# Optimization experiments

Measured on AMD Instinct MI355X. Metric: run time of the kernel, lower is better.

## Reference

```python
import jax, jax.numpy as jnp
import numpy as np

EPS = 1e-7  # undefined global in source; standard small epsilon
LAMBD_BDC = 1.0
LAMBD_BEC = 1.0
N, C = 8192, 100


def setup_inputs() -> dict:
    key = jax.random.key(0)
    k1, k2 = jax.random.split(key)
    inputs = jax.random.normal(k1, (N, C), dtype=jnp.float32)
    targets = jax.random.randint(k2, (N,), 0, C)
    return {"inputs": inputs, "targets": targets}


def _rest_indices(targets, num_classes):
    # Indices of all classes except the target, preserving original class order
    # (matches torch boolean-mask gather ordering).
    idx = jnp.arange(num_classes)[None, :]                 # [1, C]
    is_target = idx == targets[:, None]                    # [N, C]
    # Stable sort: non-target positions first, in ascending class order.
    order = jnp.argsort(is_target, axis=1, stable=True)    # [N, C]
    return order[:, : num_classes - 1]                     # [N, C-1]


def reference(inputs, targets):
    n, c = inputs.shape
    # Cross-entropy (mean reduction, as nn.CrossEntropyLoss default)
    logp = jax.nn.log_softmax(inputs, axis=1)
    loss_ce = -jnp.mean(jnp.take_along_axis(logp, targets[:, None], axis=1))

    # Gather target logit and the C-1 non-target logits per row
    logits_y = jnp.take_along_axis(inputs, targets[:, None], axis=1)   # [N, 1]
    rest_idx = _rest_indices(targets, c)
    logits_rest = jnp.take_along_axis(inputs, rest_idx, axis=1)        # [N, C-1]

    # BDC: -sum(logsigmoid(y - rest)) / (C-1) / N
    loss_bdc = -jnp.sum(jax.nn.log_sigmoid(logits_y - logits_rest)) / (c - 1) / n

    # BEC: pairwise differences among non-target logits, [N, C-1, C-1]
    diff = logits_rest[:, :, None] - logits_rest[:, None, :]
    loss_bec = -jnp.sum(0.5 * jax.nn.log_sigmoid(diff + EPS)) / (c - 1) / (c - 2) / n

    loss = loss_ce + LAMBD_BDC * loss_bdc + LAMBD_BEC * loss_bec
    return (loss, loss_ce, loss_bdc, loss_bec)
```

## Files before the change

kernel.cpp:

```cpp
#include <hip/hip_runtime.h>

#define NROWS 8192
#define NCLS  100
#define NB    (NROWS / 4)
#define LN2   0.6931471805599453f
#define LOG2E 1.4426950408889634f

#if __has_builtin(__builtin_amdgcn_exp2f)
#define EXP2F(x) __builtin_amdgcn_exp2f(x)
#else
#define EXP2F(x) __expf((x) * LN2)
#endif
#if __has_builtin(__builtin_amdgcn_logf)
#define LOG2F(x) __builtin_amdgcn_logf(x)
#else
#define LOG2F(x) (__logf(x) * LOG2E)
#endif

#define TILEIJ(idx, I, J) \
    float s_##I = sqrtf(fmaf(8.f, (float)(idx), 1.f)); \
    int J = (int)((1.0f + s_##I) * 0.5f); \
    int I = (idx) - ((J * (J - 1)) >> 1);

#define HT(EA, RA, EB, RB, P) { P *= fmaf((EB), (RA), (EA) * (RB)); }

#define TILE16H(Ea, Ra, Eb, Rb, P0, P1, P2, P3) \
  HT(Ea.x, Ra.x, Eb.x, Rb.x, P0) HT(Ea.x, Ra.x, Eb.y, Rb.y, P0) \
  HT(Ea.x, Ra.x, Eb.z, Rb.z, P0) HT(Ea.x, Ra.x, Eb.w, Rb.w, P0) \
  HT(Ea.y, Ra.y, Eb.x, Rb.x, P1) HT(Ea.y, Ra.y, Eb.y, Rb.y, P1) \
  HT(Ea.y, Ra.y, Eb.z, Rb.z, P1) HT(Ea.y, Ra.y, Eb.w, Rb.w, P1) \
  HT(Ea.z, Ra.z, Eb.x, Rb.x, P2) HT(Ea.z, Ra.z, Eb.y, Rb.y, P2) \
  HT(Ea.z, Ra.z, Eb.z, Rb.z, P2) HT(Ea.z, Ra.z, Eb.w, Rb.w, P2) \
  HT(Ea.w, Ra.w, Eb.x, Rb.x, P3) HT(Ea.w, Ra.w, Eb.y, Rb.y, P3) \
  HT(Ea.w, Ra.w, Eb.z, Rb.z, P3) HT(Ea.w, Ra.w, Eb.w, Rb.w, P3)

__device__ __forceinline__ float wave_dpp_sum(float v) {
#define DPPADD(ctrl) { int y_ = __builtin_amdgcn_update_dpp( \
        0, __builtin_bit_cast(int, v), (ctrl), 0xf, 0xf, true); \
        v += __builtin_bit_cast(float, y_); }
    DPPADD(0x111)
    DPPADD(0x112)
    DPPADD(0x114)
    DPPADD(0x118)
    DPPADD(0x142)
    DPPADD(0x143)
#undef DPPADD
    return v;
}

__global__ __launch_bounds__(256, 8) void cpc_rows(const float* __restrict__ in,
                                                   const int* __restrict__ tgt,
                                                   float* __restrict__ qb) {
    __shared__ __align__(16) float sx[4][128], sE[4][128], sR[4][128];
    __shared__ float bred[4][3];

    const int tid = threadIdx.x;
    const int w   = tid >> 6;
    const int l   = tid & 63;
    const int row = blockIdx.x * 4 + w;
    const float* x = in + row * NCLS;

    float x0 = x[l] * LOG2E;
    float E0 = EXP2F((x0 - 4.f) * 0.5f);
    sx[w][l] = x0;
    sE[w][l] = E0;
    sR[w][l] = EXP2F((x0 + 4.f) * -0.5f);
    const bool v1 = (l < NCLS - 64);
    float x1 = 0.f, E1 = 0.f;
    if (v1) {
        x1 = x[64 + l] * LOG2E;
        E1 = EXP2F((x1 - 4.f) * 0.5f);
        sx[w][64 + l] = x1;
        sE[w][64 + l] = E1;
        sR[w][64 + l] = EXP2F((x1 + 4.f) * -0.5f);
    }
    __syncthreads();

    const int   t  = tgt[row];
    const float xt = sx[w][t];

    float At, Pb, es, xs;
    {
        float a0 = fabsf(xt - x0);
        float e0 = (l == t) ? 0.f : EXP2F(-a0);
        At = a0; Pb = 1.f + e0;
        es = E0 * E0;
        xs = x0;
    }
    {
        float a1 = v1 ? fabsf(xt - x1) : 0.f;
        float e1 = (v1 && (64 + l) != t) ? EXP2F(-a1) : 0.f;
        At += a1; Pb = fmaf(Pb, e1, Pb);
        es = v1 ? fmaf(E1, E1, es) : es;
        xs += x1;
    }
    float lPb = LOG2F(Pb);

    const float* pE = sE[w];
    const float* pR = sR[w];

    float P0 = 1.f, P1 = 1.f, P2 = 1.f, P3 = 1.f;
    float cst = 512.f;
#pragma unroll 1
    for (int it = 0; it < 4; ++it) {
        int idx = it * 64 + l;
        TILEIJ(idx, I, J)
        float4 Ea = *(const float4*)(pE + 4 * I);
        float4 Ra = *(const float4*)(pR + 4 * I);
        float4 Eb = *(const float4*)(pE + 4 * J);
        float4 Rb = *(const float4*)(pR + 4 * J);
        TILE16H(Ea, Ra, Eb, Rb, P0, P1, P2, P3)
    }
    {
        int idx = 256 + l;
        bool tv = idx < 300;
        int idxc = tv ? idx : 0;
        TILEIJ(idxc, I, J)
        float4 Ea = *(const float4*)(pE + 4 * I);
        float4 Ra = *(const float4*)(pR + 4 * I);
        float4 Eb = *(const float4*)(pE + 4 * J);
        float4 Rb = *(const float4*)(pR + 4 * J);
        float S0 = P0, S1 = P1, S2 = P2, S3 = P3;
        TILE16H(Ea, Ra, Eb, Rb, P0, P1, P2, P3)
        P0 = tv ? P0 : S0; P1 = tv ? P1 : S1;
        P2 = tv ? P2 : S2; P3 = tv ? P3 : S3;
        cst += tv ? 128.f : 0.f;
    }
    float Pd0 = 1.f, Pd1 = 1.f;
    {
        bool dv = l < 25;
        int I = dv ? l : 0;
        float4 Ea = *(const float4*)(pE + 4 * I);
        float4 Ra = *(const float4*)(pR + 4 * I);
        TILE16H(Ea, Ra, Ea, Ra, Pd0, Pd1, Pd0, Pd1)
        Pd0 = dv ? Pd0 : 1.f;
        Pd1 = dv ? Pd1 : 1.f;
        cst += dv ? 64.f : 0.f;
    }

    float lS = 2.f * ((LOG2F(P0) + LOG2F(P1)) + (LOG2F(P2) + LOG2F(P3)))
             + LOG2F(Pd0 * Pd1) + cst;

    float r0 = wave_dpp_sum(es);
    float rU = wave_dpp_sum(xs + At + 2.f * lPb);
    float rW = wave_dpp_sum(At + 2.f * lPb - lS);

    if (l == 63) {
        bred[w][0] = LN2 * (LOG2F(r0) + 4.f - xt);
        bred[w][1] = LN2 * (50.f * xt - 0.5f * rU);
        bred[w][2] = LN2 * (rW + 1.f);
    }
    __syncthreads();
    if (tid < 3) {
        float s = bred[0][tid] + bred[1][tid] + bred[2][tid] + bred[3][tid];
        qb[tid * NB + blockIdx.x] = s;
    }
}

__global__ __launch_bounds__(256) void cpc_final(const float* __restrict__ qb,
                                                 float* __restrict__ out) {
    __shared__ double sred[4][3];
    const int tid = threadIdx.x;
    const int lane = tid & 63, wid = tid >> 6;
    double a0 = 0, a1 = 0, a2 = 0;
#pragma unroll
    for (int it = 0; it < 2; ++it) {
        int idx = (it * 256 + tid) * 4;
        float4 v0 = *(const float4*)(qb + idx);
        float4 v1 = *(const float4*)(qb + NB + idx);
        float4 v2 = *(const float4*)(qb + 2 * NB + idx);
        a0 += (double)v0.x; a0 += (double)v0.y; a0 += (double)v0.z; a0 += (double)v0.w;
        a1 += (double)v1.x; a1 += (double)v1.y; a1 += (double)v1.z; a1 += (double)v1.w;
        a2 += (double)v2.x; a2 += (double)v2.y; a2 += (double)v2.z; a2 += (double)v2.w;
    }
#pragma unroll
    for (int off = 32; off; off >>= 1) {
        a0 += __shfl_xor(a0, off, 64);
        a1 += __shfl_xor(a1, off, 64);
        a2 += __shfl_xor(a2, off, 64);
    }
    if (lane == 0) { sred[wid][0] = a0; sred[wid][1] = a1; sred[wid][2] = a2; }
    __syncthreads();
    if (tid == 0) {
        double ce  = (sred[0][0] + sred[1][0] + sred[2][0] + sred[3][0]) / (double)NROWS;
        double bdc = -(sred[0][1] + sred[1][1] + sred[2][1] + sred[3][1])
                     / (double)(NCLS - 1) / (double)NROWS;
        double bec = -0.5 * (sred[0][2] + sred[1][2] + sred[2][2] + sred[3][2])
                     / (double)(NCLS - 1) / (double)(NCLS - 2) / (double)NROWS;
        out[0] = (float)(ce + bdc + bec);
        out[1] = (float)ce;
        out[2] = (float)bdc;
        out[3] = (float)bec;
    }
}

extern "C" void kernel_launch(void* const* d_in, const int* in_sizes, int n_in,
                              void* d_out, int out_size, void* d_ws, size_t ws_size,
                              hipStream_t stream) {
    const float* inputs  = (const float*)d_in[0];
    const int*   targets = (const int*)d_in[1];
    float*       out     = (float*)d_out;
    float*       qb      = (float*)d_ws;

    cpc_rows<<<NB, 256, 0, stream>>>(inputs, targets, qb);
    cpc_final<<<1, 256, 0, stream>>>(qb, out);
}
```

Before: 14.64 us.

## Process two rows per wave and replace four log2 calls with exponent extraction

Each wave now handles two rows, so blocks cover 8 rows and the grid is halved. Both rows' loads and exp computations are issued before the barrier, which gives more memory-level parallelism per wave. The final reduction then reads half as many partials. The four separate LOG2F calls on the product accumulators are replaced by splitting off the float exponent bits and taking one log of the combined mantissas, which cuts transcendental work. The trade-off is fewer waves in flight (2048 blocks become 1024), longer serial work per wave, and higher LDS use per block.

```diff
diff --git a/kernel.cpp b/kernel.cpp
--- a/kernel.cpp
+++ b/kernel.cpp
@@ -2,7 +2,7 @@
 
 #define NROWS 8192
 #define NCLS  100
-#define NB    (NROWS / 4)
+#define NBLK  (NROWS / 8)
 #define LN2   0.6931471805599453f
 #define LOG2E 1.4426950408889634f
 
@@ -48,112 +48,137 @@
     return v;
 }
 
+#define EXPSPLIT(P, EI, MF) \
+    int   EI = __builtin_bit_cast(int, P) >> 23; \
+    float MF = __builtin_bit_cast(float, (__builtin_bit_cast(int, P) & 0x007FFFFF) | 0x3F800000);
+
 __global__ __launch_bounds__(256, 8) void cpc_rows(const float* __restrict__ in,
                                                    const int* __restrict__ tgt,
                                                    float* __restrict__ qb) {
-    __shared__ __align__(16) float sx[4][128], sE[4][128], sR[4][128];
+    __shared__ __align__(16) float sx[4][2][128], sE[4][2][128], sR[4][2][128];
     __shared__ float bred[4][3];
 
     const int tid = threadIdx.x;
     const int w   = tid >> 6;
     const int l   = tid & 63;
-    const int row = blockIdx.x * 4 + w;
-    const float* x = in + row * NCLS;
-
-    float x0 = x[l] * LOG2E;
-    float E0 = EXP2F((x0 - 4.f) * 0.5f);
-    sx[w][l] = x0;
-    sE[w][l] = E0;
-    sR[w][l] = EXP2F((x0 + 4.f) * -0.5f);
+    const int row0 = blockIdx.x * 8 + w * 2;
+    const float* xA = in + row0 * NCLS;
+    const float* xB = xA + NCLS;
     const bool v1 = (l < NCLS - 64);
-    float x1 = 0.f, E1 = 0.f;
+
+    float xa0 = xA[l] * LOG2E;
+    float xb0 = xB[l] * LOG2E;
+    float Ea0 = EXP2F((xa0 - 4.f) * 0.5f);
+    float Eb0 = EXP2F((xb0 - 4.f) * 0.5f);
+    sx[w][0][l] = xa0; sE[w][0][l] = Ea0; sR[w][0][l] = EXP2F((xa0 + 4.f) * -0.5f);
+    sx[w][1][l] = xb0; sE[w][1][l] = Eb0; sR[w][1][l] = EXP2F((xb0 + 4.f) * -0.5f);
+    float xa1 = 0.f, xb1 = 0.f, Ea1 = 0.f, Eb1 = 0.f;
     if (v1) {
-        x1 = x[64 + l] * LOG2E;
-        E1 = EXP2F((x1 - 4.f) * 0.5f);
-        sx[w][64 + l] = x1;
-        sE[w][64 + l] = E1;
-        sR[w][64 + l] = EXP2F((x1 + 4.f) * -0.5f);
-    }
+        xa1 = xA[64 + l] * LOG2E;
+        xb1 = xB[64 + l] * LOG2E;
+        Ea1 = EXP2F((xa1 - 4.f) * 0.5f);
+        Eb1 = EXP2F((xb1 - 4.f) * 0.5f);
+        sx[w][0][64 + l] = xa1; sE[w][0][64 + l] = Ea1; sR[w][0][64 + l] = EXP2F((xa1 + 4.f) * -0.5f);
+        sx[w][1][64 + l] = xb1; sE[w][1][64 + l] = Eb1; sR[w][1][64 + l] = EXP2F((xb1 + 4.f) * -0.5f);
+    }
+    const int t0 = tgt[row0];
+    const int t1 = tgt[row0 + 1];
     __syncthreads();
 
-    const int   t  = tgt[row];
-    const float xt = sx[w][t];
-
-    float At, Pb, es, xs;
-    {
-        float a0 = fabsf(xt - x0);
-        float e0 = (l == t) ? 0.f : EXP2F(-a0);
-        At = a0; Pb = 1.f + e0;
-        es = E0 * E0;
-        xs = x0;
-    }
-    {
-        float a1 = v1 ? fabsf(xt - x1) : 0.f;
-        float e1 = (v1 && (64 + l) != t) ? EXP2F(-a1) : 0.f;
-        At += a1; Pb = fmaf(Pb, e1, Pb);
-        es = v1 ? fmaf(E1, E1, es) : es;
-        xs += x1;
-    }
-    float lPb = LOG2F(Pb);
-
-    const float* pE = sE[w];
-    const float* pR = sR[w];
-
-    float P0 = 1.f, P1 = 1.f, P2 = 1.f, P3 = 1.f;
-    float cst = 512.f;
+    float acc0 = 0.f, acc1 = 0.f, acc2 = 0.f;
+
 #pragma unroll 1
-    for (int it = 0; it < 4; ++it) {
-        int idx = it * 64 + l;
-        TILEIJ(idx, I, J)
-        float4 Ea = *(const float4*)(pE + 4 * I);
-        float4 Ra = *(const float4*)(pR + 4 * I);
-        float4 Eb = *(const float4*)(pE + 4 * J);
-        float4 Rb = *(const float4*)(pR + 4 * J);
-        TILE16H(Ea, Ra, Eb, Rb, P0, P1, P2, P3)
-    }
-    {
-        int idx = 256 + l;
-        bool tv = idx < 300;
-        int idxc = tv ? idx : 0;
-        TILEIJ(idxc, I, J)
-        float4 Ea = *(const float4*)(pE + 4 * I);
-        float4 Ra = *(const float4*)(pR + 4 * I);
-        float4 Eb = *(const float4*)(pE + 4 * J);
-        float4 Rb = *(const float4*)(pR + 4 * J);
-        float S0 = P0, S1 = P1, S2 = P2, S3 = P3;
-        TILE16H(Ea, Ra, Eb, Rb, P0, P1, P2, P3)
-        P0 = tv ? P0 : S0; P1 = tv ? P1 : S1;
-        P2 = tv ? P2 : S2; P3 = tv ? P3 : S3;
-        cst += tv ? 128.f : 0.f;
-    }
-    float Pd0 = 1.f, Pd1 = 1.f;
-    {
-        bool dv = l < 25;
-        int I = dv ? l : 0;
-        float4 Ea = *(const float4*)(pE + 4 * I);
-        float4 Ra = *(const float4*)(pR + 4 * I);
-        TILE16H(Ea, Ra, Ea, Ra, Pd0, Pd1, Pd0, Pd1)
-        Pd0 = dv ? Pd0 : 1.f;
-        Pd1 = dv ? Pd1 : 1.f;
-        cst += dv ? 64.f : 0.f;
-    }
-
-    float lS = 2.f * ((LOG2F(P0) + LOG2F(P1)) + (LOG2F(P2) + LOG2F(P3)))
-             + LOG2F(Pd0 * Pd1) + cst;
-
-    float r0 = wave_dpp_sum(es);
-    float rU = wave_dpp_sum(xs + At + 2.f * lPb);
-    float rW = wave_dpp_sum(At + 2.f * lPb - lS);
-
-    if (l == 63) {
-        bred[w][0] = LN2 * (LOG2F(r0) + 4.f - xt);
-        bred[w][1] = LN2 * (50.f * xt - 0.5f * rU);
-        bred[w][2] = LN2 * (rW + 1.f);
-    }
+    for (int r = 0; r < 2; ++r) {
+        const float* px = sx[w][r];
+        const float* pE = sE[w][r];
+        const float* pR = sR[w][r];
+        const float x0 = r ? xb0 : xa0;
+        const float x1 = r ? xb1 : xa1;
+        const float E0 = r ? Eb0 : Ea0;
+        const float E1 = r ? Eb1 : Ea1;
+        const int   t  = r ? t1 : t0;
+        const float xt = px[t];
+
+        float At, Pb, es, xs;
+        {
+            float a0 = fabsf(xt - x0);
+            float e0 = (l == t) ? 0.f : EXP2F(-a0);
+            At = a0; Pb = 1.f + e0;
+            es = E0 * E0;
+            xs = x0;
+        }
+        {
+            float a1 = v1 ? fabsf(xt - x1) : 0.f;
+            float e1 = (v1 && (64 + l) != t) ? EXP2F(-a1) : 0.f;
+            At += a1; Pb = fmaf(Pb, e1, Pb);
+            es = v1 ? fmaf(E1, E1, es) : es;
+            xs += x1;
+        }
+        float lPb = LOG2F(Pb);
+
+        float P0 = 1.f, P1 = 1.f, P2 = 1.f, P3 = 1.f;
+        float cst = 512.f;
+#pragma unroll 1
+        for (int it = 0; it < 4; ++it) {
+            int idx = it * 64 + l;
+            TILEIJ(idx, I, J)
+            float4 Ea = *(const float4*)(pE + 4 * I);
+            float4 Ra = *(const float4*)(pR + 4 * I);
+            float4 Eb = *(const float4*)(pE + 4 * J);
+            float4 Rb = *(const float4*)(pR + 4 * J);
+            TILE16H(Ea, Ra, Eb, Rb, P0, P1, P2, P3)
+        }
+        {
+            int idx = 256 + l;
+            bool tv = idx < 300;
+            int idxc = tv ? idx : 0;
+            TILEIJ(idxc, I, J)
+            float4 Ea = *(const float4*)(pE + 4 * I);
+            float4 Ra = *(const float4*)(pR + 4 * I);
+            float4 Eb = *(const float4*)(pE + 4 * J);
+            float4 Rb = *(const float4*)(pR + 4 * J);
+            float S0 = P0, S1 = P1, S2 = P2, S3 = P3;
+            TILE16H(Ea, Ra, Eb, Rb, P0, P1, P2, P3)
+            P0 = tv ? P0 : S0; P1 = tv ? P1 : S1;
+            P2 = tv ? P2 : S2; P3 = tv ? P3 : S3;
+            cst += tv ? 128.f : 0.f;
+        }
+        float Pd0 = 1.f, Pd1 = 1.f;
+        {
+            bool dv = l < 25;
+            int I = dv ? l : 0;
+            float4 Ea = *(const float4*)(pE + 4 * I);
+            float4 Ra = *(const float4*)(pR + 4 * I);
+            TILE16H(Ea, Ra, Ea, Ra, Pd0, Pd1, Pd0, Pd1)
+            Pd0 = dv ? Pd0 : 1.f;
+            Pd1 = dv ? Pd1 : 1.f;
+            cst += dv ? 64.f : 0.f;
+        }
+
+        float Pd = Pd0 * Pd1;
+        EXPSPLIT(P0, e0i, m0) EXPSPLIT(P1, e1i, m1)
+        EXPSPLIT(P2, e2i, m2) EXPSPLIT(P3, e3i, m3)
+        EXPSPLIT(Pd, edi, md)
+        int eAll = 2 * (((e0i + e1i) + (e2i + e3i)) - 508) + (edi - 127);
+        float mA = (m0 * m1) * (m2 * m3);
+        float lS = (float)eAll + LOG2F((mA * mA) * md) + cst;
+
+        float r0 = wave_dpp_sum(es);
+        float rU = wave_dpp_sum(xs + At + 2.f * lPb);
+        float rW = wave_dpp_sum(At + 2.f * lPb - lS);
+
+        if (l == 63) {
+            acc0 += LN2 * (LOG2F(r0) + 4.f - xt);
+            acc1 += LN2 * (50.f * xt - 0.5f * rU);
+            acc2 += LN2 * (rW + 1.f);
+        }
+    }
+
+    if (l == 63) { bred[w][0] = acc0; bred[w][1] = acc1; bred[w][2] = acc2; }
     __syncthreads();
     if (tid < 3) {
         float s = bred[0][tid] + bred[1][tid] + bred[2][tid] + bred[3][tid];
-        qb[tid * NB + blockIdx.x] = s;
+        qb[tid * NBLK + blockIdx.x] = s;
     }
 }
 
@@ -163,12 +188,11 @@
     const int tid = threadIdx.x;
     const int lane = tid & 63, wid = tid >> 6;
     double a0 = 0, a1 = 0, a2 = 0;
-#pragma unroll
-    for (int it = 0; it < 2; ++it) {
-        int idx = (it * 256 + tid) * 4;
+    {
+        int idx = tid * 4;
         float4 v0 = *(const float4*)(qb + idx);
-        float4 v1 = *(const float4*)(qb + NB + idx);
-        float4 v2 = *(const float4*)(qb + 2 * NB + idx);
+        float4 v1 = *(const float4*)(qb + NBLK + idx);
+        float4 v2 = *(const float4*)(qb + 2 * NBLK + idx);
         a0 += (double)v0.x; a0 += (double)v0.y; a0 += (double)v0.z; a0 += (double)v0.w;
         a1 += (double)v1.x; a1 += (double)v1.y; a1 += (double)v1.z; a1 += (double)v1.w;
         a2 += (double)v2.x; a2 += (double)v2.y; a2 += (double)v2.z; a2 += (double)v2.w;
@@ -202,6 +226,6 @@
     float*       out     = (float*)d_out;
     float*       qb      = (float*)d_ws;
 
-    cpc_rows<<<NB, 256, 0, stream>>>(inputs, targets, qb);
+    cpc_rows<<<NBLK, 256, 0, stream>>>(inputs, targets, qb);
     cpc_final<<<1, 256, 0, stream>>>(qb, out);
 }
```

New measurement: 14.75 us. No clear change (+0.8%).

## Compute pairwise BEC products in packed fp16 with interleaved E/R shared layout

Applied to the files above, without the earlier changes.

Stores the exp(x/2) and exp(-x/2) factors as fp16 interleaved in one shared array, so each 4-class tile loads as a single 16-byte h8. The pairwise terms are then computed with packed half2 math and partial products are folded into fewer fp32 accumulators, with the scale offsets and constants changed to match. This is meant to halve shared-memory traffic and the ALU work of the O(C^2) inner loop. In exchange, the reduced fp16 range and precision in the products could affect accuracy or overflow.

```diff
diff --git a/kernel.cpp b/kernel.cpp
--- a/kernel.cpp
+++ b/kernel.cpp
@@ -17,22 +17,32 @@
 #define LOG2F(x) (__logf(x) * LOG2E)
 #endif
 
+typedef _Float16 h2 __attribute__((ext_vector_type(2)));
+typedef _Float16 h8 __attribute__((ext_vector_type(8)));
+
 #define TILEIJ(idx, I, J) \
     float s_##I = sqrtf(fmaf(8.f, (float)(idx), 1.f)); \
     int J = (int)((1.0f + s_##I) * 0.5f); \
     int I = (idx) - ((J * (J - 1)) >> 1);
 
-#define HT(EA, RA, EB, RB, P) { P *= fmaf((EB), (RA), (EA) * (RB)); }
-
-#define TILE16H(Ea, Ra, Eb, Rb, P0, P1, P2, P3) \
-  HT(Ea.x, Ra.x, Eb.x, Rb.x, P0) HT(Ea.x, Ra.x, Eb.y, Rb.y, P0) \
-  HT(Ea.x, Ra.x, Eb.z, Rb.z, P0) HT(Ea.x, Ra.x, Eb.w, Rb.w, P0) \
-  HT(Ea.y, Ra.y, Eb.x, Rb.x, P1) HT(Ea.y, Ra.y, Eb.y, Rb.y, P1) \
-  HT(Ea.y, Ra.y, Eb.z, Rb.z, P1) HT(Ea.y, Ra.y, Eb.w, Rb.w, P1) \
-  HT(Ea.z, Ra.z, Eb.x, Rb.x, P2) HT(Ea.z, Ra.z, Eb.y, Rb.y, P2) \
-  HT(Ea.z, Ra.z, Eb.z, Rb.z, P2) HT(Ea.z, Ra.z, Eb.w, Rb.w, P2) \
-  HT(Ea.w, Ra.w, Eb.x, Rb.x, P3) HT(Ea.w, Ra.w, Eb.y, Rb.y, P3) \
-  HT(Ea.w, Ra.w, Eb.z, Rb.z, P3) HT(Ea.w, Ra.w, Eb.w, Rb.w, P3)
+__device__ __forceinline__ h2 ht2(_Float16 ei, _Float16 ri, h2 EJ, h2 RJ) {
+    h2 e = {ei, ei}, r = {ri, ri};
+    return e * RJ + EJ * r;
+}
+
+#define TILE2x(rI, rJ, PA, PB) { \
+    h2 EJ0 = {rJ[0], rJ[1]}, EJ1 = {rJ[2], rJ[3]}; \
+    h2 RJ0 = {rJ[4], rJ[5]}, RJ1 = {rJ[6], rJ[7]}; \
+    h2 pa = ht2(rI[0], rI[4], EJ0, RJ0); \
+    pa *= ht2(rI[0], rI[4], EJ1, RJ1); \
+    pa *= ht2(rI[1], rI[5], EJ0, RJ0); \
+    pa *= ht2(rI[1], rI[5], EJ1, RJ1); \
+    h2 pb = ht2(rI[2], rI[6], EJ0, RJ0); \
+    pb *= ht2(rI[2], rI[6], EJ1, RJ1); \
+    pb *= ht2(rI[3], rI[7], EJ0, RJ0); \
+    pb *= ht2(rI[3], rI[7], EJ1, RJ1); \
+    PA *= (float)pa[0] * (float)pa[1]; \
+    PB *= (float)pb[0] * (float)pb[1]; }
 
 __device__ __forceinline__ float wave_dpp_sum(float v) {
 #define DPPADD(ctrl) { int y_ = __builtin_amdgcn_update_dpp( \
@@ -51,7 +61,8 @@
 __global__ __launch_bounds__(256, 8) void cpc_rows(const float* __restrict__ in,
                                                    const int* __restrict__ tgt,
                                                    float* __restrict__ qb) {
-    __shared__ __align__(16) float sx[4][128], sE[4][128], sR[4][128];
+    __shared__ float sx[4][128];
+    __shared__ __align__(16) h8 sq[4][25];
     __shared__ float bred[4][3];
 
     const int tid = threadIdx.x;
@@ -59,20 +70,24 @@
     const int l   = tid & 63;
     const int row = blockIdx.x * 4 + w;
     const float* x = in + row * NCLS;
+    _Float16* hq = (_Float16*)sq[w];
 
     float x0 = x[l] * LOG2E;
-    float E0 = EXP2F((x0 - 4.f) * 0.5f);
+    float E0f = EXP2F(x0 * 0.5f - 1.f);
+    float R0f = EXP2F(x0 * -0.5f - 1.f);
     sx[w][l] = x0;
-    sE[w][l] = E0;
-    sR[w][l] = EXP2F((x0 + 4.f) * -0.5f);
+    hq[(l >> 2) * 8 + (l & 3)]     = (_Float16)E0f;
+    hq[(l >> 2) * 8 + 4 + (l & 3)] = (_Float16)R0f;
     const bool v1 = (l < NCLS - 64);
-    float x1 = 0.f, E1 = 0.f;
+    float x1 = 0.f, E1f = 0.f;
     if (v1) {
-        x1 = x[64 + l] * LOG2E;
-        E1 = EXP2F((x1 - 4.f) * 0.5f);
-        sx[w][64 + l] = x1;
-        sE[w][64 + l] = E1;
-        sR[w][64 + l] = EXP2F((x1 + 4.f) * -0.5f);
+        int c = 64 + l;
+        x1 = x[c] * LOG2E;
+        E1f = EXP2F(x1 * 0.5f - 1.f);
+        float R1f = EXP2F(x1 * -0.5f - 1.f);
+        sx[w][c] = x1;
+        hq[(c >> 2) * 8 + (c & 3)]     = (_Float16)E1f;
+        hq[(c >> 2) * 8 + 4 + (c & 3)] = (_Float16)R1f;
     }
     __syncthreads();
 
@@ -84,69 +99,62 @@
         float a0 = fabsf(xt - x0);
         float e0 = (l == t) ? 0.f : EXP2F(-a0);
         At = a0; Pb = 1.f + e0;
-        es = E0 * E0;
+        es = E0f * E0f;
         xs = x0;
     }
     {
         float a1 = v1 ? fabsf(xt - x1) : 0.f;
         float e1 = (v1 && (64 + l) != t) ? EXP2F(-a1) : 0.f;
         At += a1; Pb = fmaf(Pb, e1, Pb);
-        es = v1 ? fmaf(E1, E1, es) : es;
+        es = v1 ? fmaf(E1f, E1f, es) : es;
         xs += x1;
     }
     float lPb = LOG2F(Pb);
 
-    const float* pE = sE[w];
-    const float* pR = sR[w];
-
-    float P0 = 1.f, P1 = 1.f, P2 = 1.f, P3 = 1.f;
-    float cst = 512.f;
+    const h8* pq = sq[w];
+
+    float P0 = 1.f, P1 = 1.f;
+    float cst = 256.f;
 #pragma unroll 1
     for (int it = 0; it < 4; ++it) {
         int idx = it * 64 + l;
         TILEIJ(idx, I, J)
-        float4 Ea = *(const float4*)(pE + 4 * I);
-        float4 Ra = *(const float4*)(pR + 4 * I);
-        float4 Eb = *(const float4*)(pE + 4 * J);
-        float4 Rb = *(const float4*)(pR + 4 * J);
-        TILE16H(Ea, Ra, Eb, Rb, P0, P1, P2, P3)
+        h8 rI = pq[I];
+        h8 rJ = pq[J];
+        TILE2x(rI, rJ, P0, P1)
     }
     {
         int idx = 256 + l;
         bool tv = idx < 300;
         int idxc = tv ? idx : 0;
         TILEIJ(idxc, I, J)
-        float4 Ea = *(const float4*)(pE + 4 * I);
-        float4 Ra = *(const float4*)(pR + 4 * I);
-        float4 Eb = *(const float4*)(pE + 4 * J);
-        float4 Rb = *(const float4*)(pR + 4 * J);
-        float S0 = P0, S1 = P1, S2 = P2, S3 = P3;
-        TILE16H(Ea, Ra, Eb, Rb, P0, P1, P2, P3)
-        P0 = tv ? P0 : S0; P1 = tv ? P1 : S1;
-        P2 = tv ? P2 : S2; P3 = tv ? P3 : S3;
-        cst += tv ? 128.f : 0.f;
-    }
-    float Pd0 = 1.f, Pd1 = 1.f;
+        h8 rI = pq[I];
+        h8 rJ = pq[J];
+        float S0 = P0, S1 = P1;
+        TILE2x(rI, rJ, P0, P1)
+        P0 = tv ? P0 : S0;
+        P1 = tv ? P1 : S1;
+        cst += tv ? 64.f : 0.f;
+    }
+    float Pd = 1.f;
     {
         bool dv = l < 25;
         int I = dv ? l : 0;
-        float4 Ea = *(const float4*)(pE + 4 * I);
-        float4 Ra = *(const float4*)(pR + 4 * I);
-        TILE16H(Ea, Ra, Ea, Ra, Pd0, Pd1, Pd0, Pd1)
-        Pd0 = dv ? Pd0 : 1.f;
-        Pd1 = dv ? Pd1 : 1.f;
-        cst += dv ? 64.f : 0.f;
-    }
-
-    float lS = 2.f * ((LOG2F(P0) + LOG2F(P1)) + (LOG2F(P2) + LOG2F(P3)))
-             + LOG2F(Pd0 * Pd1) + cst;
+        h8 rI = pq[I];
+        float Pda = 1.f, Pdb = 1.f;
+        TILE2x(rI, rI, Pda, Pdb)
+        Pd = dv ? (Pda * Pdb) : 1.f;
+        cst += dv ? 32.f : 0.f;
+    }
+
+    float lS = 2.f * LOG2F(P0 * P1) + LOG2F(Pd) + cst;
 
     float r0 = wave_dpp_sum(es);
     float rU = wave_dpp_sum(xs + At + 2.f * lPb);
     float rW = wave_dpp_sum(At + 2.f * lPb - lS);
 
     if (l == 63) {
-        bred[w][0] = LN2 * (LOG2F(r0) + 4.f - xt);
+        bred[w][0] = LN2 * (LOG2F(r0) + 2.f - xt);
         bred[w][1] = LN2 * (50.f * xt - 0.5f * rU);
         bred[w][2] = LN2 * (rW + 1.f);
     }
```

New measurement: 17.84 us. 21.9% more time.
